# Kernel tuning notes

Measured on AMD Instinct MI355X. Metric: run time of the kernel, lower is better.

The kernel has to match this reference:

```python
import jax, jax.numpy as jnp
import numpy as np

B, N, C = 4, 3136, 64
IMG_H = IMG_W = 56
HEADS = 1
TOPK = 8
HID = 4 * C  # mlp_ratio=4.0


def _ln(x, g, b, eps=1e-5):
    m = x.mean(-1, keepdims=True)
    v = ((x - m) ** 2).mean(-1, keepdims=True)
    return (x - m) * jax.lax.rsqrt(v + eps) * g + b


def _conv(x, w, b, pad, groups):
    y = jax.lax.conv_general_dilated(
        x, w, (1, 1), [(pad, pad), (pad, pad)],
        dimension_numbers=('NCHW', 'OIHW', 'NCHW'), feature_group_count=groups)
    return y + b[None, :, None, None]


def setup_inputs() -> dict:
    key = jax.random.key(0)
    ks = jax.random.split(key, 10)
    def rn(k, shp, scale=0.02):
        return jax.random.normal(k, shp, jnp.float32) * scale
    return {
        'x': jax.random.normal(ks[0], (B, N, C), jnp.float32),
        'norm1_g': jnp.ones((C,), jnp.float32), 'norm1_b': jnp.zeros((C,), jnp.float32),
        'wq': rn(ks[1], (C, C)), 'bq': jnp.zeros((C,), jnp.float32),
        'wkv': rn(ks[2], (C, 2 * C)), 'bkv': jnp.zeros((2 * C,), jnp.float32),
        'wproj': rn(ks[3], (C, C)), 'bproj': jnp.zeros((C,), jnp.float32),
        'local_w': rn(ks[4], (C, C // HEADS, 3, 3), 0.05), 'local_b': jnp.zeros((C,), jnp.float32),
        'norm2_g': jnp.ones((C,), jnp.float32), 'norm2_b': jnp.zeros((C,), jnp.float32),
        'w3': rn(ks[5], (HID, 1, 3, 3), 0.05), 'b3': jnp.zeros((HID,), jnp.float32),
        'w5': rn(ks[6], (HID, 1, 5, 5), 0.05), 'b5': jnp.zeros((HID,), jnp.float32),
        'w1': rn(ks[7], (C, 2 * HID, 1, 1), 0.05), 'b1': jnp.zeros((C,), jnp.float32),
        'H': IMG_H, 'W': IMG_W,
    }


def reference(x, norm1_g, norm1_b, wq, bq, wkv, bkv, wproj, bproj,
              local_w, local_b, norm2_g, norm2_b, w3, b3, w5, b5, w1, b1, H, W):
    Bb, Nn, Cc = x.shape
    d = Cc // HEADS
    scale = d ** -0.5
    # --- DynamicSparseAttention (global branch) ---
    xn = _ln(x, norm1_g, norm1_b)
    q = (xn @ wq + bq).reshape(Bb, Nn, HEADS, d).transpose(0, 2, 1, 3)       # bhnd
    kv = (xn @ wkv + bkv).reshape(Bb, Nn, 2, HEADS, d)
    k = kv[:, :, 0].transpose(0, 2, 1, 3)
    v = kv[:, :, 1].transpose(0, 2, 1, 3)
    attn = jnp.einsum('bhnd,bhmd->bhnm', q, k) * scale                        # [B,h,N,N]
    kth = jax.lax.top_k(attn, TOPK)[0][..., -1:]                              # k-th largest per row
    mask = (attn >= kth).astype(attn.dtype)                                   # top-k scatter mask
    p = jax.nn.softmax(attn * mask, axis=-1)                                  # zeros kept (as in torch ref)
    g = jnp.einsum('bhnm,bhmd->bhnd', p, v).transpose(0, 2, 1, 3).reshape(Bb, Nn, Cc)
    g = g @ wproj + bproj
    # --- local conv attention branch ---
    x_img = x.transpose(0, 2, 1).reshape(Bb, Cc, H, W)
    loc = _conv(x_img, local_w, local_b, 1, HEADS).reshape(Bb, Cc, Nn).transpose(0, 2, 1)
    # --- residual 1 (note: norm1 params reused, as in source) ---
    x = x + _ln(g + loc, norm1_g, norm1_b)
    # --- MSFN ---
    xn2 = _ln(x, norm2_g, norm2_b).transpose(0, 2, 1).reshape(Bb, Cc, H, W)
    x3 = _conv(xn2, w3, b3, 1, Cc)   # depthwise 3x3, channel mult 4
    x5 = _conv(xn2, w5, b5, 2, Cc)   # depthwise 5x5, channel mult 4
    m = _conv(jnp.concatenate([x3, x5], axis=1), w1, b1, 0, 1)
    return x + m.reshape(Bb, Cc, Nn).transpose(0, 2, 1)
```

## Files before the change

kernel.cpp:

```cpp
#include <hip/hip_runtime.h>
#include <math.h>

#define Bv 4
#define Nv 3136
#define Cv 64
#define Hh 56
#define Ww 56
#define HIDv 256
#define TOPKv 8
#define TSP 520
#define LCP 584
#define XNP 72
#define KSPL 16
#define KPS 196

constexpr float SCALE = 0.125f;
constexpr float EPS = 1e-5f;
constexpr float SBIAS = 128.0f;

typedef short bf16x8 __attribute__((ext_vector_type(8)));
typedef float f32x4 __attribute__((ext_vector_type(4)));

#define CSWAP(a, b) { unsigned int _hi = max(a, b); unsigned int _lo = min(a, b); a = _hi; b = _lo; }
#define BITONIC8(T) \
  CSWAP(T[0], T[4]); CSWAP(T[1], T[5]); CSWAP(T[2], T[6]); CSWAP(T[3], T[7]); \
  CSWAP(T[0], T[2]); CSWAP(T[1], T[3]); CSWAP(T[4], T[6]); CSWAP(T[5], T[7]); \
  CSWAP(T[0], T[1]); CSWAP(T[2], T[3]); CSWAP(T[4], T[5]); CSWAP(T[6], T[7]);

__device__ __forceinline__ unsigned short f2bf(float f) {
  unsigned int u = __float_as_uint(f);
  u = (u + 0x7FFFu + ((u >> 16) & 1u)) >> 16;
  return (unsigned short)u;
}
__device__ __forceinline__ float bf2f(unsigned short u) {
  return __uint_as_float(((unsigned int)u) << 16);
}
__device__ __forceinline__ unsigned int pack2(float a, float b) {
  return (unsigned int)f2bf(a) | ((unsigned int)f2bf(b) << 16);
}

__device__ __forceinline__ unsigned int packB(float sb, int j) {
  return (__float_as_uint(sb) & 0xFFFFF000u) | (unsigned int)j;
}

__global__ void k_transpose(const float* __restrict__ w1, const float* __restrict__ lw,
                            const float* __restrict__ w3, const float* __restrict__ w5,
                            const float* __restrict__ wq, const float* __restrict__ wkv,
                            const float* __restrict__ bq, const float* __restrict__ bkv,
                            const float* __restrict__ wproj,
                            unsigned short* __restrict__ w1bf, unsigned short* __restrict__ lwb,
                            float* __restrict__ w3t, float* __restrict__ w5t,
                            unsigned short* __restrict__ wqkvt, float* __restrict__ qkvb,
                            unsigned short* __restrict__ wprojt, float* __restrict__ sumv) {
  int p = blockIdx.x * 256 + threadIdx.x;
  if (p < 256) sumv[p] = 0.0f;
  if (p < 64 * 512) w1bf[p] = f2bf(w1[p]);
  if (p < 64 * 576) {
    int co = p / 576, k = p % 576;
    int tap = k >> 6, ci = k & 63;
    lwb[p] = f2bf(lw[co * 576 + ci * 9 + tap]);
  }
  if (p < 36 * 64) {
    int cin = p & 63, tm = p >> 6;
    int tap = tm >> 2, m = tm & 3;
    w3t[p] = w3[(cin * 4 + m) * 9 + tap];
  }
  if (p < 100 * 64) {
    int cin = p & 63, tm = p >> 6;
    int tap = tm >> 2, m = tm & 3;
    w5t[p] = w5[(cin * 4 + m) * 25 + tap];
  }
  if (p < 192 * 64) {
    int o = p >> 6, i = p & 63;
    float v = (o < 64) ? wq[i * 64 + o] : wkv[i * 128 + (o - 64)];
    wqkvt[p] = f2bf(v);
  }
  if (p < 192) qkvb[p] = (p < 64) ? bq[p] : bkv[p - 64];
  if (p < 64 * 64) {
    int o = p >> 6, i = p & 63;
    wprojt[p] = f2bf(wproj[i * 64 + o]);
  }
}

__global__ __launch_bounds__(256) void k_ln_qkv(
    const float* __restrict__ x, const float* __restrict__ g1, const float* __restrict__ b1,
    const unsigned short* __restrict__ wqkvt, const float* __restrict__ qkvb,
    unsigned short* __restrict__ q16, unsigned short* __restrict__ k16,
    float* __restrict__ vo, float* __restrict__ sumv) {
  __shared__ __align__(16) unsigned short xnS[16 * XNP];
  int bid = blockIdx.x;
  int b = bid / 196, tile = bid % 196;
  size_t tok0 = (size_t)b * Nv + tile * 16;
  int t = threadIdx.x;
  int w = t >> 6, l = t & 63;
  int tokL = t >> 4;
  int ch0 = (t & 15) * 4;
  size_t tok = tok0 + tokL;
  float v[4];
  *(float4*)v = *(const float4*)&x[tok * 64 + ch0];
  float s = v[0] + v[1] + v[2] + v[3];
  float s2 = v[0] * v[0] + v[1] * v[1] + v[2] * v[2] + v[3] * v[3];
#pragma unroll
  for (int off = 1; off <= 8; off <<= 1) {
    s += __shfl_xor(s, off, 64);
    s2 += __shfl_xor(s2, off, 64);
  }
  float m = s * (1.f / 64.f);
  float rs = rsqrtf(s2 * (1.f / 64.f) - m * m + EPS);
  {
    unsigned int pk[2];
    float a0_ = (v[0] - m) * rs * g1[ch0] + b1[ch0];
    float a1_ = (v[1] - m) * rs * g1[ch0 + 1] + b1[ch0 + 1];
    float a2_ = (v[2] - m) * rs * g1[ch0 + 2] + b1[ch0 + 2];
    float a3_ = (v[3] - m) * rs * g1[ch0 + 3] + b1[ch0 + 3];
    pk[0] = pack2(a0_, a1_);
    pk[1] = pack2(a2_, a3_);
    *(uint2*)&xnS[tokL * XNP + ch0] = *(uint2*)pk;
  }
  __syncthreads();
  int n = l & 15, q = l >> 4;
  const bf16x8 a0 = *(const bf16x8*)&xnS[n * XNP + q * 8];
  const bf16x8 a1 = *(const bf16x8*)&xnS[n * XNP + 32 + q * 8];
  {
    const unsigned short* wr = &wqkvt[(size_t)(w * 16 + n) * 64];
    bf16x8 b0 = *(const bf16x8*)&wr[q * 8];
    bf16x8 b1_ = *(const bf16x8*)&wr[32 + q * 8];
    f32x4 acc = {0.f, 0.f, 0.f, 0.f};
    acc = __builtin_amdgcn_mfma_f32_16x16x32_bf16(a0, b0, acc, 0, 0, 0);
    acc = __builtin_amdgcn_mfma_f32_16x16x32_bf16(a1, b1_, acc, 0, 0, 0);
    float bias = qkvb[w * 16 + n];
#pragma unroll
    for (int r = 0; r < 4; ++r)
      q16[(tok0 + q * 4 + r) * 64 + w * 16 + n] = f2bf(acc[r] + bias);
  }
  {
    const unsigned short* wr = &wqkvt[(size_t)((w + 4) * 16 + n) * 64];
    bf16x8 b0 = *(const bf16x8*)&wr[q * 8];
    bf16x8 b1_ = *(const bf16x8*)&wr[32 + q * 8];
    f32x4 acc = {0.f, 0.f, 0.f, 0.f};
    acc = __builtin_amdgcn_mfma_f32_16x16x32_bf16(a0, b0, acc, 0, 0, 0);
    acc = __builtin_amdgcn_mfma_f32_16x16x32_bf16(a1, b1_, acc, 0, 0, 0);
    float bias = qkvb[64 + w * 16 + n];
#pragma unroll
    for (int r = 0; r < 4; ++r)
      k16[(tok0 + q * 4 + r) * 64 + w * 16 + n] = f2bf(acc[r] + bias);
  }
  {
    const unsigned short* wr = &wqkvt[(size_t)((w + 8) * 16 + n) * 64];
    bf16x8 b0 = *(const bf16x8*)&wr[q * 8];
    bf16x8 b1_ = *(const bf16x8*)&wr[32 + q * 8];
    f32x4 acc = {0.f, 0.f, 0.f, 0.f};
    acc = __builtin_amdgcn_mfma_f32_16x16x32_bf16(a0, b0, acc, 0, 0, 0);
    acc = __builtin_amdgcn_mfma_f32_16x16x32_bf16(a1, b1_, acc, 0, 0, 0);
    float bias = qkvb[128 + w * 16 + n];
    float vp = acc[0] + acc[1] + acc[2] + acc[3] + 4.0f * bias;
#pragma unroll
    for (int r = 0; r < 4; ++r)
      vo[(tok0 + q * 4 + r) * 64 + w * 16 + n] = acc[r] + bias;
    vp += __shfl_xor(vp, 16, 64);
    vp += __shfl_xor(vp, 32, 64);
    if (q == 0) atomicAdd(&sumv[b * 64 + w * 16 + n], vp);
  }
}

#define PAIRMERGE(T, accA, accB, jb) { \
    unsigned int _p0 = packB(accA[0], (jb) + 0); \
    unsigned int _p1 = packB(accA[1], (jb) + 1); \
    unsigned int _p2 = packB(accA[2], (jb) + 2); \
    unsigned int _p3 = packB(accA[3], (jb) + 3); \
    unsigned int _q0 = packB(accB[0], (jb) + 16); \
    unsigned int _q1 = packB(accB[1], (jb) + 17); \
    unsigned int _q2 = packB(accB[2], (jb) + 18); \
    unsigned int _q3 = packB(accB[3], (jb) + 19); \
    CSWAP(_p0, _p1); CSWAP(_p2, _p3); CSWAP(_p0, _p2); CSWAP(_p1, _p3); CSWAP(_p1, _p2); \
    CSWAP(_q0, _q1); CSWAP(_q2, _q3); CSWAP(_q0, _q2); CSWAP(_q1, _q3); CSWAP(_q1, _q2); \
    unsigned int _u8[8] = {_p0, _p1, _p2, _p3, _q3, _q2, _q1, _q0}; \
    BITONIC8(_u8); \
    T[0] = max(T[0], _u8[7]); \
    T[1] = max(T[1], _u8[6]); \
    T[2] = max(T[2], _u8[5]); \
    T[3] = max(T[3], _u8[4]); \
    T[4] = max(T[4], _u8[3]); \
    T[5] = max(T[5], _u8[2]); \
    T[6] = max(T[6], _u8[1]); \
    T[7] = max(T[7], _u8[0]); \
    BITONIC8(T); }

__global__ __launch_bounds__(128, 3) void k_attn_topk(
    const unsigned short* __restrict__ q16, const unsigned short* __restrict__ k16,
    unsigned int* __restrict__ top8out) {
  int bid = blockIdx.x;
  int w = threadIdx.x >> 6;
  int lane = threadIdx.x & 63;
  int split = ((bid & 7) << 1) | w;
  int lin = bid >> 3;
  int b = lin / 49, tg = lin % 49;
  int qbase = b * Nv + tg * 64;
  size_t bN = (size_t)b * Nv;
  int qcol = lane & 15, quad = lane >> 4;
  int quad4 = quad * 4;

  bf16x8 qf0a[4], qf1a[4];
#pragma unroll
  for (int tt = 0; tt < 4; ++tt) {
    qf0a[tt] = *(const bf16x8*)&q16[((size_t)(qbase + tt * 16 + qcol)) * 64 + quad * 8];
    qf1a[tt] = *(const bf16x8*)&q16[((size_t)(qbase + tt * 16 + qcol)) * 64 + 32 + quad * 8];
  }

  unsigned int t8[4][8];
#pragma unroll
  for (int tt = 0; tt < 4; ++tt)
#pragma unroll
    for (int u = 0; u < 8; ++u) t8[tt][u] = 0u;

  int kbase = split * KPS;
  int m = lane & 15;
  const char* kbp = (const char*)(k16 + bN * 64);
  unsigned int offA = (unsigned int)((kbase + m) * 128 + quad * 16);
  int jbA = kbase + quad4;

  bf16x8 ka0 = *(const bf16x8*)(kbp + offA);
  bf16x8 ka1 = *(const bf16x8*)(kbp + offA + 64);
  bf16x8 kb0 = *(const bf16x8*)(kbp + offA + 2048);
  bf16x8 kb1 = *(const bf16x8*)(kbp + offA + 2112);
  offA += 4096;

#pragma unroll 1
  for (int it = 0; it < 5; ++it) {
    bf16x8 ca0 = ka0, ca1 = ka1, cb0 = kb0, cb1 = kb1;
    ka0 = *(const bf16x8*)(kbp + offA);
    ka1 = *(const bf16x8*)(kbp + offA + 64);
    kb0 = *(const bf16x8*)(kbp + offA + 2048);
    kb1 = *(const bf16x8*)(kbp + offA + 2112);
    offA += 4096;

#pragma unroll
    for (int tt = 0; tt < 4; ++tt) {
      f32x4 accA = {SBIAS, SBIAS, SBIAS, SBIAS};
      accA = __builtin_amdgcn_mfma_f32_16x16x32_bf16(ca0, qf0a[tt], accA, 0, 0, 0);
      accA = __builtin_amdgcn_mfma_f32_16x16x32_bf16(ca1, qf1a[tt], accA, 0, 0, 0);
      f32x4 accB = {SBIAS, SBIAS, SBIAS, SBIAS};
      accB = __builtin_amdgcn_mfma_f32_16x16x32_bf16(cb0, qf0a[tt], accB, 0, 0, 0);
      accB = __builtin_amdgcn_mfma_f32_16x16x32_bf16(cb1, qf1a[tt], accB, 0, 0, 0);
      PAIRMERGE(t8[tt], accA, accB, jbA);
    }
    jbA += 32;
  }

  {
    bf16x8 ca0 = ka0, ca1 = ka1, cb0 = kb0, cb1 = kb1;
    ka0 = *(const bf16x8*)(kbp + offA);
    ka1 = *(const bf16x8*)(kbp + offA + 64);

#pragma unroll
    for (int tt = 0; tt < 4; ++tt) {
      f32x4 accA = {SBIAS, SBIAS, SBIAS, SBIAS};
      accA = __builtin_amdgcn_mfma_f32_16x16x32_bf16(ca0, qf0a[tt], accA, 0, 0, 0);
      accA = __builtin_amdgcn_mfma_f32_16x16x32_bf16(ca1, qf1a[tt], accA, 0, 0, 0);
      f32x4 accB = {SBIAS, SBIAS, SBIAS, SBIAS};
      accB = __builtin_amdgcn_mfma_f32_16x16x32_bf16(cb0, qf0a[tt], accB, 0, 0, 0);
      accB = __builtin_amdgcn_mfma_f32_16x16x32_bf16(cb1, qf1a[tt], accB, 0, 0, 0);
      PAIRMERGE(t8[tt], accA, accB, jbA);
    }
    jbA += 32;
  }

  {
    bool val = quad == 0;
#pragma unroll
    for (int tt = 0; tt < 4; ++tt) {
      f32x4 accA = {SBIAS, SBIAS, SBIAS, SBIAS};
      accA = __builtin_amdgcn_mfma_f32_16x16x32_bf16(ka0, qf0a[tt], accA, 0, 0, 0);
      accA = __builtin_amdgcn_mfma_f32_16x16x32_bf16(ka1, qf1a[tt], accA, 0, 0, 0);
      unsigned int p0 = val ? packB(accA[0], jbA + 0) : 0u;
      unsigned int p1 = val ? packB(accA[1], jbA + 1) : 0u;
      unsigned int p2 = val ? packB(accA[2], jbA + 2) : 0u;
      unsigned int p3 = val ? packB(accA[3], jbA + 3) : 0u;
      CSWAP(p0, p1); CSWAP(p2, p3); CSWAP(p0, p2); CSWAP(p1, p3); CSWAP(p1, p2);
      t8[tt][4] = max(t8[tt][4], p3);
      t8[tt][5] = max(t8[tt][5], p2);
      t8[tt][6] = max(t8[tt][6], p1);
      t8[tt][7] = max(t8[tt][7], p0);
      BITONIC8(t8[tt]);
    }
  }

#pragma unroll
  for (int tt = 0; tt < 4; ++tt) {
#pragma unroll
    for (int step = 16; step <= 32; step <<= 1) {
      unsigned int o[8];
#pragma unroll
      for (int i = 0; i < 8; ++i) o[i] = (unsigned int)__shfl_xor((int)t8[tt][i], step, 64);
      unsigned int nw[8];
#pragma unroll
      for (int i = 0; i < 8; ++i) nw[i] = max(t8[tt][i], o[7 - i]);
#pragma unroll
      for (int i = 0; i < 8; ++i) t8[tt][i] = nw[i];
      BITONIC8(t8[tt]);
    }
    if (quad == 0) {
      size_t obase = ((size_t)(bN + tg * 64 + tt * 16 + qcol)) * 128 + split * 8;
      *(uint4*)&top8out[obase] = make_uint4(t8[tt][0], t8[tt][1], t8[tt][2], t8[tt][3]);
      *(uint4*)&top8out[obase + 4] = make_uint4(t8[tt][4], t8[tt][5], t8[tt][6], t8[tt][7]);
    }
  }
}

__global__ __launch_bounds__(256) void k_attn_proj(
    const unsigned int* __restrict__ top8, const float* __restrict__ vg,
    const float* __restrict__ sumv, const float* __restrict__ x,
    const unsigned short* __restrict__ lwb, const float* __restrict__ lb,
    const unsigned short* __restrict__ wprojt, const float* __restrict__ bproj,
    const float* __restrict__ g1, const float* __restrict__ b1,
    const float* __restrict__ g2, const float* __restrict__ b2,
    float* __restrict__ x2, unsigned short* __restrict__ xn2b) {
  __shared__ float kwS[16][8];
  __shared__ int kidxS[16][8];
  __shared__ float invZS[16];
  __shared__ __align__(16) unsigned short imS[16 * LCP];
  __shared__ __align__(16) unsigned short gS[16 * XNP];
  __shared__ float yS[16 * 66];
  int bid = blockIdx.x;
  int b = bid / 196, rem = bid % 196;
  int th = rem / 7, tw = rem % 7;
  int h0 = th * 2, w0 = tw * 8;
  size_t bN = (size_t)b * Nv;
  int t = threadIdx.x;

  for (int p = t; p < 1152; p += 256) {
    int sub = p & 7, s = p >> 3;
    int tok = s / 9, tap = s % 9;
    int tr = tok >> 3, tc = tok & 7;
    int dh = tap / 3, dw = tap % 3;
    int gh = h0 + tr - 1 + dh, gw = w0 + tc - 1 + dw;
    uint4 uu = {0u, 0u, 0u, 0u};
    if (gh >= 0 && gh < Hh && gw >= 0 && gw < Ww) {
      const float* xp = &x[(bN + gh * Ww + gw) * 64 + sub * 8];
      float4 va = *(const float4*)xp;
      float4 vb = *(const float4*)(xp + 4);
      uu.x = pack2(va.x, va.y);
      uu.y = pack2(va.z, va.w);
      uu.z = pack2(vb.x, vb.y);
      uu.w = pack2(vb.z, vb.w);
    }
    *(uint4*)&imS[tok * LCP + tap * 64 + sub * 8] = uu;
  }

  if (t < 16) {
    int gtok = (h0 + (t >> 3)) * Ww + w0 + (t & 7);
    size_t base = (bN + gtok) * 128;
    unsigned int A[8];
#pragma unroll
    for (int i = 0; i < 8; ++i) A[i] = top8[base + i];
#pragma unroll
    for (int h = 1; h < 16; ++h) {
      unsigned int Bb[8];
#pragma unroll
      for (int i = 0; i < 8; ++i) Bb[i] = top8[base + h * 8 + i];
#pragma unroll
      for (int i = 0; i < 8; ++i) A[i] = max(A[i], Bb[7 - i]);
      BITONIC8(A);
    }
    float Z = (float)(Nv - TOPKv);
#pragma unroll
    for (int u = 0; u < 8; ++u) {
      float sb = __uint_as_float(A[u] & 0xFFFFF000u);
      float s = (sb - SBIAS) * SCALE;
      float e = __expf(s);
      kwS[t][u] = e - 1.0f;
      kidxS[t][u] = (int)(A[u] & 0xFFFu);
      Z += e;
    }
    invZS[t] = 1.0f / Z;
  }
  __syncthreads();

  int w = t >> 6, l = t & 63;
  int n = l & 15, q = l >> 4;

  f32x4 lacc = {0.f, 0.f, 0.f, 0.f};
  {
    const unsigned short* lwrow = &lwb[(size_t)(w * 16 + n) * 576];
#pragma unroll 6
    for (int kk = 0; kk < 18; ++kk) {
      bf16x8 af = *(const bf16x8*)&imS[n * LCP + kk * 32 + q * 8];
      bf16x8 bfr = *(const bf16x8*)&lwrow[kk * 32 + q * 8];
      lacc = __builtin_amdgcn_mfma_f32_16x16x32_bf16(af, bfr, lacc, 0, 0, 0);
    }
  }
  float lbias = lb[w * 16 + n];

  {
    int c = t & 63, rg = t >> 6;
    float sv = sumv[b * 64 + c];
#pragma unroll
    for (int rr = 0; rr < 4; ++rr) {
      int tokL = rg * 4 + rr;
      float acc = sv;
#pragma unroll
      for (int u = 0; u < 8; ++u)
        acc += kwS[tokL][u] * vg[(bN + kidxS[tokL][u]) * 64 + c];
      gS[tokL * XNP + c] = f2bf(acc * invZS[tokL]);
    }
  }
  __syncthreads();

  {
    const bf16x8 a0 = *(const bf16x8*)&gS[n * XNP + q * 8];
    const bf16x8 a1 = *(const bf16x8*)&gS[n * XNP + 32 + q * 8];
    const unsigned short* wr = &wprojt[(size_t)(w * 16 + n) * 64];
    bf16x8 b0 = *(const bf16x8*)&wr[q * 8];
    bf16x8 b1_ = *(const bf16x8*)&wr[32 + q * 8];
    f32x4 acc = {0.f, 0.f, 0.f, 0.f};
    acc = __builtin_amdgcn_mfma_f32_16x16x32_bf16(a0, b0, acc, 0, 0, 0);
    acc = __builtin_amdgcn_mfma_f32_16x16x32_bf16(a1, b1_, acc, 0, 0, 0);
    float bias = bproj[w * 16 + n];
#pragma unroll
    for (int r = 0; r < 4; ++r)
      yS[(q * 4 + r) * 66 + w * 16 + n] = acc[r] + bias + lacc[r] + lbias;
  }
  __syncthreads();

  int tokL = t >> 4;
  int ch0 = (t & 15) * 4;
  size_t tok = bN + (size_t)(h0 + (tokL >> 3)) * Ww + w0 + (tokL & 7);
  float y[4];
#pragma unroll
  for (int i = 0; i < 4; ++i) y[i] = yS[tokL * 66 + ch0 + i];
  float s = y[0] + y[1] + y[2] + y[3];
  float s2 = y[0] * y[0] + y[1] * y[1] + y[2] * y[2] + y[3] * y[3];
#pragma unroll
  for (int off = 1; off <= 8; off <<= 1) {
    s += __shfl_xor(s, off, 64);
    s2 += __shfl_xor(s2, off, 64);
  }
  float m1 = s * (1.f / 64.f);
  float rs1 = rsqrtf(s2 * (1.f / 64.f) - m1 * m1 + EPS);
  float xv[4];
  *(float4*)xv = *(const float4*)&x[tok * 64 + ch0];
  float x2v[4];
  float t_s = 0.f, t_s2 = 0.f;
#pragma unroll
  for (int i = 0; i < 4; ++i) {
    float t1 = (y[i] - m1) * rs1 * g1[ch0 + i] + b1[ch0 + i];
    x2v[i] = xv[i] + t1;
    t_s += x2v[i];
    t_s2 += x2v[i] * x2v[i];
  }
#pragma unroll
  for (int off = 1; off <= 8; off <<= 1) {
    t_s += __shfl_xor(t_s, off, 64);
    t_s2 += __shfl_xor(t_s2, off, 64);
  }
  float m2 = t_s * (1.f / 64.f);
  float rs2 = rsqrtf(t_s2 * (1.f / 64.f) - m2 * m2 + EPS);
  *(float4*)&x2[tok * 64 + ch0] = *(float4*)x2v;
  unsigned int pk[2];
  {
    float a0_ = (x2v[0] - m2) * rs2 * g2[ch0] + b2[ch0];
    float a1_ = (x2v[1] - m2) * rs2 * g2[ch0 + 1] + b2[ch0 + 1];
    float a2_ = (x2v[2] - m2) * rs2 * g2[ch0 + 2] + b2[ch0 + 2];
    float a3_ = (x2v[3] - m2) * rs2 * g2[ch0 + 3] + b2[ch0 + 3];
    pk[0] = pack2(a0_, a1_);
    pk[1] = pack2(a2_, a3_);
  }
  *(uint2*)&xn2b[tok * 64 + ch0] = *(uint2*)pk;
}

__global__ __launch_bounds__(256) void k_msfn(
    const unsigned short* __restrict__ xn2b, const float* __restrict__ x2,
    const float* __restrict__ w3t, const float* __restrict__ b3,
    const float* __restrict__ w5t, const float* __restrict__ b5,
    const unsigned short* __restrict__ w1bf, const float* __restrict__ b1,
    float* __restrict__ out) {
  __shared__ __align__(16) unsigned short xtS[6 * 12 * 64];
  __shared__ __align__(16) unsigned short tsS[16 * TSP];

  int bid = blockIdx.x;
  int b = bid / 196;
  int rem = bid % 196;
  int th = rem / 7, tw = rem % 7;
  int h0 = th * 2, w0 = tw * 8;
  size_t bN = (size_t)b * Nv;
  int t = threadIdx.x;

  unsigned int* xtU = (unsigned int*)xtS;
  for (int p = t; p < 6 * 12 * 32; p += 256) {
    int cp = p & 31, rc = p >> 5;
    int r = rc / 12, cc = rc % 12;
    int gh = h0 - 2 + r, gw = w0 - 2 + cc;
    unsigned int v = 0;
    if (gh >= 0 && gh < Hh && gw >= 0 && gw < Ww)
      v = *(const unsigned int*)&xn2b[(bN + gh * Ww + gw) * 64 + cp * 2];
    xtU[rc * 32 + cp] = v;
  }
  __syncthreads();

  int cin = t & 63, tg = t >> 6;
  int tr = tg >> 1, tc0 = (tg & 1) * 4;
  float win[5][8];
#pragma unroll
  for (int r = 0; r < 5; ++r)
#pragma unroll
    for (int c = 0; c < 8; ++c)
      win[r][c] = bf2f(xtS[((tr + r) * 12 + tc0 + c) * 64 + cin]);

  unsigned int* tsU = (unsigned int*)tsS;
#pragma unroll 1
  for (int m2 = 0; m2 < 4; m2 += 2) {
    float a3[2][9], a5[2][25], bb3[2], bb5[2];
#pragma unroll
    for (int mm = 0; mm < 2; ++mm) {
      int m = m2 + mm;
#pragma unroll
      for (int tap = 0; tap < 9; ++tap) a3[mm][tap] = w3t[(tap * 4 + m) * 64 + cin];
#pragma unroll
      for (int tap = 0; tap < 25; ++tap) a5[mm][tap] = w5t[(tap * 4 + m) * 64 + cin];
      bb3[mm] = b3[cin * 4 + m];
      bb5[mm] = b5[cin * 4 + m];
    }
#pragma unroll
    for (int tk = 0; tk < 4; ++tk) {
      int tok = tg * 4 + tk;
      unsigned int p3 = 0, p5 = 0;
#pragma unroll
      for (int mm = 0; mm < 2; ++mm) {
        float acc3 = bb3[mm];
#pragma unroll
        for (int kh = 0; kh < 3; ++kh)
#pragma unroll
          for (int kw2 = 0; kw2 < 3; ++kw2)
            acc3 += win[1 + kh][tk + 1 + kw2] * a3[mm][kh * 3 + kw2];
        float acc5 = bb5[mm];
#pragma unroll
        for (int kh = 0; kh < 5; ++kh)
#pragma unroll
          for (int kw2 = 0; kw2 < 5; ++kw2)
            acc5 += win[kh][tk + kw2] * a5[mm][kh * 5 + kw2];
        p3 |= (unsigned int)f2bf(acc3) << (16 * mm);
        p5 |= (unsigned int)f2bf(acc5) << (16 * mm);
      }
      tsU[(tok * TSP + cin * 4 + m2) >> 1] = p3;
      tsU[(tok * TSP + 256 + cin * 4 + m2) >> 1] = p5;
    }
  }
  __syncthreads();

  int wv = tg, lane = t & 63;
  int n16 = lane & 15, quad = lane >> 4;
  const unsigned short* wrow = &w1bf[(size_t)(wv * 16 + n16) * 512];
  f32x4 acc = {0.f, 0.f, 0.f, 0.f};
#pragma unroll 4
  for (int kk = 0; kk < 16; ++kk) {
    bf16x8 af = *(const bf16x8*)&tsS[n16 * TSP + kk * 32 + quad * 8];
    bf16x8 bfr = *(const bf16x8*)&wrow[kk * 32 + quad * 8];
    acc = __builtin_amdgcn_mfma_f32_16x16x32_bf16(af, bfr, acc, 0, 0, 0);
  }
  float bias = b1[wv * 16 + n16];
#pragma unroll
  for (int r = 0; r < 4; ++r) {
    int tok = quad * 4 + r;
    int trr = tok >> 3, tcc = tok & 7;
    size_t idx = (bN + (size_t)(h0 + trr) * Ww + w0 + tcc) * 64 + wv * 16 + n16;
    out[idx] = x2[idx] + acc[r] + bias;
  }
}

extern "C" void kernel_launch(void* const* d_in, const int* in_sizes, int n_in,
                              void* d_out, int out_size, void* d_ws, size_t ws_size,
                              hipStream_t stream) {
  const float* x = (const float*)d_in[0];
  const float* n1g = (const float*)d_in[1];
  const float* n1b = (const float*)d_in[2];
  const float* wq = (const float*)d_in[3];
  const float* bq = (const float*)d_in[4];
  const float* wkv = (const float*)d_in[5];
  const float* bkv = (const float*)d_in[6];
  const float* wproj = (const float*)d_in[7];
  const float* bproj = (const float*)d_in[8];
  const float* lw = (const float*)d_in[9];
  const float* lb = (const float*)d_in[10];
  const float* n2g = (const float*)d_in[11];
  const float* n2b = (const float*)d_in[12];
  const float* w3 = (const float*)d_in[13];
  const float* b3 = (const float*)d_in[14];
  const float* w5 = (const float*)d_in[15];
  const float* b5 = (const float*)d_in[16];
  const float* w1 = (const float*)d_in[17];
  const float* b1 = (const float*)d_in[18];
  float* out = (float*)d_out;

  float* ws = (float*)d_ws;
  const size_t TOK = (size_t)Bv * Nv * Cv;
  float* vb = ws;
  float* sumv = vb + TOK;
  float* x2 = sumv + 256;
  float* w3t = x2 + TOK;
  float* w5t = w3t + 2304;
  float* qkvb = w5t + 6400;
  unsigned short* q16 = (unsigned short*)(qkvb + 192);
  unsigned short* k16 = q16 + TOK;
  unsigned short* xn2b = k16 + TOK;
  unsigned short* w1bf = xn2b + TOK;
  unsigned short* lwb = w1bf + 64 * 512;
  unsigned short* wqkvt = lwb + 64 * 576;
  unsigned short* wprojt = wqkvt + 192 * 64;
  unsigned int* top8ws = (unsigned int*)(wprojt + 64 * 64 + 64);

  k_transpose<<<144, 256, 0, stream>>>(w1, lw, w3, w5, wq, wkv, bq, bkv, wproj,
                                       w1bf, lwb, w3t, w5t, wqkvt, qkvb, wprojt, sumv);
  k_ln_qkv<<<Bv * 196, 256, 0, stream>>>(x, n1g, n1b, wqkvt, qkvb, q16, k16, vb, sumv);
  k_attn_topk<<<Bv * 49 * 8, 128, 0, stream>>>(q16, k16, top8ws);
  k_attn_proj<<<Bv * 196, 256, 0, stream>>>(top8ws, vb, sumv, x, lwb, lb, wprojt, bproj,
                                            n1g, n1b, n2g, n2b, x2, xn2b);
  k_msfn<<<Bv * 196, 256, 0, stream>>>(xn2b, x2, w3t, b3, w5t, b5, w1bf, b1, out);
}
```

Baseline: 172.1 us.

## Split top-k merge across lanes, overlap with im2col load, prefetch gathered V

The per-token merge of 16 partial top-8 lists now runs on 4 lanes per token, each merging 4 lists, followed by a two-step shuffle merge. Previously 16 threads did the whole merge serially. The remaining threads fill the im2col tile at the same time instead of before the merge. The gathered V rows are loaded into registers before the local-conv MFMA so their latency overlaps that compute. The tail-block validity mask in the scoring kernel also changes from a quad==0 test to an explicit index bound, which looks like a correctness adjustment.

```diff
diff --git a/kernel.cpp b/kernel.cpp
--- a/kernel.cpp
+++ b/kernel.cpp
@@ -266,16 +266,16 @@
   }
 
   {
-    bool val = quad == 0;
+    int klim = kbase + KPS;
 #pragma unroll
     for (int tt = 0; tt < 4; ++tt) {
       f32x4 accA = {SBIAS, SBIAS, SBIAS, SBIAS};
       accA = __builtin_amdgcn_mfma_f32_16x16x32_bf16(ka0, qf0a[tt], accA, 0, 0, 0);
       accA = __builtin_amdgcn_mfma_f32_16x16x32_bf16(ka1, qf1a[tt], accA, 0, 0, 0);
-      unsigned int p0 = val ? packB(accA[0], jbA + 0) : 0u;
-      unsigned int p1 = val ? packB(accA[1], jbA + 1) : 0u;
-      unsigned int p2 = val ? packB(accA[2], jbA + 2) : 0u;
-      unsigned int p3 = val ? packB(accA[3], jbA + 3) : 0u;
+      unsigned int p0 = (jbA + 0 < klim) ? packB(accA[0], jbA + 0) : 0u;
+      unsigned int p1 = (jbA + 1 < klim) ? packB(accA[1], jbA + 1) : 0u;
+      unsigned int p2 = (jbA + 2 < klim) ? packB(accA[2], jbA + 2) : 0u;
+      unsigned int p3 = (jbA + 3 < klim) ? packB(accA[3], jbA + 3) : 0u;
       CSWAP(p0, p1); CSWAP(p2, p3); CSWAP(p0, p2); CSWAP(p1, p3); CSWAP(p1, p2);
       t8[tt][4] = max(t8[tt][4], p3);
       t8[tt][5] = max(t8[tt][5], p2);
@@ -328,33 +328,15 @@
   size_t bN = (size_t)b * Nv;
   int t = threadIdx.x;
 
-  for (int p = t; p < 1152; p += 256) {
-    int sub = p & 7, s = p >> 3;
-    int tok = s / 9, tap = s % 9;
-    int tr = tok >> 3, tc = tok & 7;
-    int dh = tap / 3, dw = tap % 3;
-    int gh = h0 + tr - 1 + dh, gw = w0 + tc - 1 + dw;
-    uint4 uu = {0u, 0u, 0u, 0u};
-    if (gh >= 0 && gh < Hh && gw >= 0 && gw < Ww) {
-      const float* xp = &x[(bN + gh * Ww + gw) * 64 + sub * 8];
-      float4 va = *(const float4*)xp;
-      float4 vb = *(const float4*)(xp + 4);
-      uu.x = pack2(va.x, va.y);
-      uu.y = pack2(va.z, va.w);
-      uu.z = pack2(vb.x, vb.y);
-      uu.w = pack2(vb.z, vb.w);
-    }
-    *(uint4*)&imS[tok * LCP + tap * 64 + sub * 8] = uu;
-  }
-
-  if (t < 16) {
-    int gtok = (h0 + (t >> 3)) * Ww + w0 + (t & 7);
-    size_t base = (bN + gtok) * 128;
+  if (t < 64) {
+    int tk = t >> 2, la = t & 3;
+    int gtok = (h0 + (tk >> 3)) * Ww + w0 + (tk & 7);
+    size_t base = (bN + gtok) * 128 + la * 32;
     unsigned int A[8];
 #pragma unroll
     for (int i = 0; i < 8; ++i) A[i] = top8[base + i];
 #pragma unroll
-    for (int h = 1; h < 16; ++h) {
+    for (int h = 1; h < 4; ++h) {
       unsigned int Bb[8];
 #pragma unroll
       for (int i = 0; i < 8; ++i) Bb[i] = top8[base + h * 8 + i];
@@ -362,22 +344,62 @@
       for (int i = 0; i < 8; ++i) A[i] = max(A[i], Bb[7 - i]);
       BITONIC8(A);
     }
-    float Z = (float)(Nv - TOPKv);
-#pragma unroll
-    for (int u = 0; u < 8; ++u) {
-      float sb = __uint_as_float(A[u] & 0xFFFFF000u);
-      float s = (sb - SBIAS) * SCALE;
-      float e = __expf(s);
-      kwS[t][u] = e - 1.0f;
-      kidxS[t][u] = (int)(A[u] & 0xFFFu);
-      Z += e;
-    }
-    invZS[t] = 1.0f / Z;
+#pragma unroll
+    for (int step = 1; step <= 2; step <<= 1) {
+      unsigned int o[8];
+#pragma unroll
+      for (int i = 0; i < 8; ++i) o[i] = (unsigned int)__shfl_xor((int)A[i], step, 64);
+#pragma unroll
+      for (int i = 0; i < 8; ++i) A[i] = max(A[i], o[7 - i]);
+      BITONIC8(A);
+    }
+    if (la == 0) {
+      float Z = (float)(Nv - TOPKv);
+#pragma unroll
+      for (int u = 0; u < 8; ++u) {
+        float sb = __uint_as_float(A[u] & 0xFFFFF000u);
+        float s = (sb - SBIAS) * SCALE;
+        float e = __expf(s);
+        kwS[tk][u] = e - 1.0f;
+        kidxS[tk][u] = (int)(A[u] & 0xFFFu);
+        Z += e;
+      }
+      invZS[tk] = 1.0f / Z;
+    }
+  } else {
+    for (int p = t - 64; p < 1152; p += 192) {
+      int sub = p & 7, s = p >> 3;
+      int tok = s / 9, tap = s % 9;
+      int tr = tok >> 3, tc = tok & 7;
+      int dh = tap / 3, dw = tap % 3;
+      int gh = h0 + tr - 1 + dh, gw = w0 + tc - 1 + dw;
+      uint4 uu = {0u, 0u, 0u, 0u};
+      if (gh >= 0 && gh < Hh && gw >= 0 && gw < Ww) {
+        const float* xp = &x[(bN + gh * Ww + gw) * 64 + sub * 8];
+        float4 va = *(const float4*)xp;
+        float4 vb = *(const float4*)(xp + 4);
+        uu.x = pack2(va.x, va.y);
+        uu.y = pack2(va.z, va.w);
+        uu.z = pack2(vb.x, vb.y);
+        uu.w = pack2(vb.z, vb.w);
+      }
+      *(uint4*)&imS[tok * LCP + tap * 64 + sub * 8] = uu;
+    }
   }
   __syncthreads();
 
   int w = t >> 6, l = t & 63;
   int n = l & 15, q = l >> 4;
+
+  int c = t & 63, rg = t >> 6;
+  float vgv[4][8];
+#pragma unroll
+  for (int rr = 0; rr < 4; ++rr) {
+    int tokL = rg * 4 + rr;
+#pragma unroll
+    for (int u = 0; u < 8; ++u)
+      vgv[rr][u] = vg[(bN + kidxS[tokL][u]) * 64 + c];
+  }
 
   f32x4 lacc = {0.f, 0.f, 0.f, 0.f};
   {
@@ -392,7 +414,6 @@
   float lbias = lb[w * 16 + n];
 
   {
-    int c = t & 63, rg = t >> 6;
     float sv = sumv[b * 64 + c];
 #pragma unroll
     for (int rr = 0; rr < 4; ++rr) {
@@ -400,7 +421,7 @@
       float acc = sv;
 #pragma unroll
       for (int u = 0; u < 8; ++u)
-        acc += kwS[tokL][u] * vg[(bN + kidxS[tokL][u]) * 64 + c];
+        acc += kwS[tokL][u] * vgv[rr][u];
       gS[tokL * XNP + c] = f2bf(acc * invZS[tokL]);
     }
   }
```

New measurement: 171.1 us. No clear change (-0.6%).
